# Optimization experiments

Hardware: AMD Instinct MI355X
Metric: run time of the kernel (lower is better)

Reference implementation:

```python
import jax, jax.numpy as jnp
import numpy as np
import math

L_DEG, N_PTS, T_ER, P_RAD, C_IN, C_OUT = 4, 8192, 15, 5, 16, 16


def _cg(j1, m1, j2, m2, j3, m3):
    # Clebsch-Gordan coefficient <j1 m1 j2 m2 | j3 m3> (Racah formula),
    # replacing sympy's CG(...).doit() used by the original module.
    if m1 + m2 != m3:
        return 0.0
    if j3 < abs(j1 - j2) or j3 > j1 + j2:
        return 0.0
    f = math.factorial
    pre = math.sqrt((2 * j3 + 1) * f(j3 + j1 - j2) * f(j3 - j1 + j2) * f(j1 + j2 - j3) / f(j1 + j2 + j3 + 1))
    pre *= math.sqrt(f(j3 + m3) * f(j3 - m3) * f(j1 - m1) * f(j1 + m1) * f(j2 - m2) * f(j2 + m2))
    s = 0.0
    for k in range(max(0, j2 - j3 - m1, j1 - j3 + m2), min(j1 + j2 - j3, j1 - m1, j2 + m2) + 1):
        s += (-1.0) ** k / (f(k) * f(j1 + j2 - j3 - k) * f(j1 - m1 - k) * f(j2 + m2 - k) * f(j3 - j2 + m1 + k) * f(j3 - j1 - m2 + k))
    return pre * s


def _precompute(L):
    # Mirrors PrecomputingTensorsForConv6D.
    tens, coefs = [], []
    for l in range(L):
        for l1 in range(L):
            for l2 in range(abs(l - l1), min(L, l + l1 + 1)):
                coefs.append(8.0 * np.pi ** 2 / (2 * l1 + 1)
                             * np.sqrt((2 * l + 1) * (2 * l1 + 1) / (4.0 * np.pi * (2 * l2 + 1)))
                             * _cg(l, 0, l1, 0, l2, 0))
                T1 = np.zeros((l + 1, l1 + 1, l2 + 1), np.float32)
                T2 = np.zeros_like(T1)
                T3 = np.zeros_like(T1)
                for k in range(l + 1):
                    for k1 in range(l1 + 1):
                        if k + k1 < l2 + 1:
                            T1[k, k1, k + k1] = _cg(l, k, l1, k1, l2, k + k1) * (-1) ** k1
                        if k1 > 0 and abs(k - k1) < l2 + 1:
                            if k - k1 >= 0:
                                T2[k, k1, k - k1] = _cg(l, k, l1, -k1, l2, k - k1) * (-1) ** l1
                            else:
                                T3[k, k1, k1 - k] = (-1) ** (k1 - k) * (-1) ** (l1 + l2) * _cg(l, k, l1, -k1, l2, k - k1)
                tens += [T1, T2, T3]
    return tens, [float(c) for c in coefs]


_TENS_NP, _COEFS = _precompute(L_DEG)
_TENS = [jnp.asarray(t, jnp.float32) for t in _TENS_NP]


def _forward(xs, ws, bs):
    L = L_DEG
    # zero the imaginary k=0 rows, as done via temp_term in build()
    ws_m = list(ws)
    bs_m = list(bs)
    for l in range(L):
        mk = (jnp.arange(l + 1) > 0).astype(jnp.float32)
        ws_m[2 * l + 1] = ws[2 * l + 1] * mk[:, None, None, None, None]
        bs_m[2 * l + 1] = bs[2 * l + 1] * mk[None, :, None, None]
    out = []
    itr = 0
    for l in range(L):
        o_r = 0.0
        o_i = 0.0
        for l1 in range(L):
            wr, wi = ws_m[2 * l1], ws_m[2 * l1 + 1]
            for l2 in range(abs(l - l1), min(L, l + l1 + 1)):
                c = _COEFS[itr]
                T1, T2, T3 = _TENS[3 * itr], _TENS[3 * itr + 1], _TENS[3 * itr + 2]
                xr, xi = xs[2 * l2], xs[2 * l2 + 1]
                # x: [n, t, k(l2+1), p, i]; w: [m(l1+1), t, p, i, j]; T: [l(l+1), m, k]
                o_r = o_r + c * jnp.einsum('lmk,ntkpi,mtpij->nlpj', T1 + T2 + T3, xr, wr) \
                          - c * jnp.einsum('lmk,ntkpi,mtpij->nlpj', T1 - T2 + T3, xi, wi)
                o_i = o_i + c * jnp.einsum('lmk,ntkpi,mtpij->nlpj', T1 - T2 - T3, xr, wi) \
                          + c * jnp.einsum('lmk,ntkpi,mtpij->nlpj', T1 + T2 - T3, xi, wr)
                itr += 1
        out.append(o_r + bs_m[2 * l])
        out.append(o_i + bs_m[2 * l + 1])
    return tuple(out)


def setup_inputs() -> dict:
    key = jax.random.key(0)
    ks = jax.random.split(key, 24)
    inp = {}
    i = 0
    for l in range(L_DEG):
        for part in ('r', 'i'):
            inp['x%d%s' % (l, part)] = jax.random.normal(ks[i], (N_PTS, T_ER, l + 1, P_RAD, C_IN), jnp.float32)
            i += 1
    for l in range(L_DEG):
        for part in ('r', 'i'):
            inp['w%d%s' % (l, part)] = jax.random.normal(ks[i], (l + 1, T_ER, P_RAD, C_IN, C_OUT), jnp.float32) * 0.05
            i += 1
    for l in range(L_DEG):
        for part in ('r', 'i'):
            inp['b%d%s' % (l, part)] = jax.random.normal(ks[i], (1, l + 1, P_RAD, C_OUT), jnp.float32) * 0.05
            i += 1
    return inp


def reference(x0r, x0i, x1r, x1i, x2r, x2i, x3r, x3i,
              w0r, w0i, w1r, w1i, w2r, w2i, w3r, w3i,
              b0r, b0i, b1r, b1i, b2r, b2i, b3r, b3i):
    xs = [x0r, x0i, x1r, x1i, x2r, x2i, x3r, x3i]
    ws = [w0r, w0i, w1r, w1i, w2r, w2i, w3r, w3i]
    bs = [b0r, b0i, b1r, b1i, b2r, b2i, b3r, b3i]
    return _forward(xs, ws, bs)
```

## Files before the change

### kernel.cpp

```cpp
#include <hip/hip_runtime.h>

#define PI_D 3.14159265358979323846


typedef __attribute__((ext_vector_type(8))) short short8;
typedef __attribute__((ext_vector_type(4))) float f32x4;

struct Ptrs8 { const float* p[8]; };

__device__ __forceinline__ ushort f2bf(float x){
  uint u = __float_as_uint(x);
  return (ushort)((u + 0x7fffu + ((u>>16)&1u)) >> 16);
}

__device__ __forceinline__ double dfact(int n){ double r=1.0; for(int i=2;i<=n;++i) r*=(double)i; return r; }

__device__ double cg_coef(int j1,int m1,int j2,int m2,int j3,int m3){
  if(m1+m2!=m3) return 0.0;
  if(j3<abs(j1-j2)||j3>j1+j2) return 0.0;
  if(abs(m1)>j1||abs(m2)>j2||abs(m3)>j3) return 0.0;
  double pre = sqrt((2.0*j3+1.0)*dfact(j3+j1-j2)*dfact(j3-j1+j2)*dfact(j1+j2-j3)/dfact(j1+j2+j3+1));
  pre *= sqrt(dfact(j3+m3)*dfact(j3-m3)*dfact(j1-m1)*dfact(j1+m1)*dfact(j2-m2)*dfact(j2+m2));
  int kmin = max(0,max(j2-j3-m1,j1-j3+m2));
  int kmax = min(j1+j2-j3,min(j1-m1,j2+m2));
  double s=0.0;
  for(int k=kmin;k<=kmax;++k){
    double d = dfact(k)*dfact(j1+j2-j3-k)*dfact(j1-m1-k)*dfact(j2+m2-k)*dfact(j3-j2+m1+k)*dfact(j3-j1-m2+k);
    s += ((k&1)?-1.0:1.0)/d;
  }
  return pre*s;
}

__device__ __forceinline__ int gidx(int l,int l2,int combo,int lr,int kx,int l1,int m){
  return ((((((l*4+l2)*4+combo)*4+lr)*4+kx)*4+l1)*4+m);
}

__global__ void g_kernel(float* __restrict__ G){
  int tid = threadIdx.x;
  for(int e=tid;e<16384;e+=blockDim.x) G[e]=0.0f;
  __syncthreads();
  int trip = tid >> 4;
  int sub  = tid & 15;
  int lr = sub >> 2, m = sub & 3;
  int idx=0;
  for(int l=0;l<4;l++)for(int l1=0;l1<4;l1++){
    int lo=abs(l-l1), hi=min(3,l+l1);
    for(int l2=lo;l2<=hi;l2++){
      if(idx==trip && lr<=l && m<=l1){
        double c = 8.0*PI_D*PI_D/(2.0*l1+1.0)
                 * sqrt((2.0*l+1.0)*(2.0*l1+1.0)/(4.0*PI_D*(2.0*l2+1.0)))
                 * cg_coef(l,0,l1,0,l2,0);
        if(lr+m<=l2){
          float f = (float)(c * cg_coef(l,lr,l1,m,l2,lr+m) * ((m&1)?-1.0:1.0));
          G[gidx(l,l2,0,lr,lr+m,l1,m)] += f;
          G[gidx(l,l2,1,lr,lr+m,l1,m)] -= f;
          G[gidx(l,l2,2,lr,lr+m,l1,m)] += f;
          G[gidx(l,l2,3,lr,lr+m,l1,m)] += f;
        }
        if(m>0 && abs(lr-m)<=l2){
          if(lr-m>=0){
            float f = (float)(c * cg_coef(l,lr,l1,-m,l2,lr-m) * ((l1&1)?-1.0:1.0));
            G[gidx(l,l2,0,lr,lr-m,l1,m)] += f;
            G[gidx(l,l2,1,lr,lr-m,l1,m)] += f;
            G[gidx(l,l2,2,lr,lr-m,l1,m)] -= f;
            G[gidx(l,l2,3,lr,lr-m,l1,m)] += f;
          } else {
            float f = (float)(c * (((m-lr)&1)?-1.0:1.0) * (((l1+l2)&1)?-1.0:1.0)
                              * cg_coef(l,lr,l1,-m,l2,lr-m));
            G[gidx(l,l2,0,lr,m-lr,l1,m)] += f;
            G[gidx(l,l2,1,lr,m-lr,l1,m)] -= f;
            G[gidx(l,l2,2,lr,m-lr,l1,m)] -= f;
            G[gidx(l,l2,3,lr,m-lr,l1,m)] -= f;
          }
        }
      }
      idx++;
    }
  }
}

__device__ __forceinline__ void decode_kb(int kb,int& l2,int& partp,int& kx,int& t){
  int kbo;
  if(kb<30){l2=0;kbo=0;} else if(kb<90){l2=1;kbo=30;} else if(kb<180){l2=2;kbo=90;} else {l2=3;kbo=180;}
  int rem = kb-kbo;
  int per = (l2+1)*15;
  partp = rem/per;
  int q = rem%per;
  kx = q/15; t = q%15;
}

__device__ __forceinline__ void decode_col(int col,int& l,int& part,int& lr,int& j){
  int co;
  if(col<32){l=0;co=0;} else if(col<96){l=1;co=32;} else if(col<192){l=2;co=96;} else {l=3;co=192;}
  int cr = col-co; int per=(l+1)*16;
  part = cr/per; int q = cr%per; lr = q>>4; j = q&15;
}

__global__ void w_kernel(const float* __restrict__ G, Ptrs8 wp, ushort* __restrict__ W){
  long e = (long)blockIdx.x*256 + threadIdx.x;
  if(e >= 5L*320*4800) return;
  int K = (int)(e%4800); long r = e/4800; int col = (int)(r%320); int p = (int)(r/320);
  int i = K & 15; int kb = K >> 4;
  int l2,partp,kx,t; decode_kb(kb,l2,partp,kx,t);
  int l,part,lr,j; decode_col(col,l,part,lr,j);
  int combo = (part==0) ? (partp==0?0:1) : (partp==0?2:3);
  int wpart = (combo==0||combo==3)?0:1;
  int mstart = wpart?1:0;
  int woff = t*1280 + p*256 + i*16 + j;
  float acc=0.f;
  for(int l1=0;l1<4;l1++){
    const float* wptr = wp.p[l1*2+wpart];
    int gb = ((((l*4+l2)*4+combo)*4+lr)*4+kx)*16 + l1*4;
    for(int m=mstart;m<=l1;m++){
      float g = G[gb+m];
      if(g!=0.f) acc += g * wptr[m*19200 + woff];
    }
  }
  W[e] = f2bf(acc);
}


__device__ __forceinline__ void a_load(const Ptrs8& xp, int p, int n0, int kt, int w, int lane, float4* v){
  int kb = kt*4 + w;
  int l2,partp,kx,t; decode_kb(kb,l2,partp,kx,t);
  const float* xb = xp.p[l2*2+partp];
  int nstr = 1200*(l2+1);
  const float* base = xb + (long)(n0 + (lane>>2))*nstr + (t*(l2+1)+kx)*80 + p*16 + (lane&3)*4;
  long step = (long)16*nstr;
  #pragma unroll
  for(int s=0;s<4;++s) v[s] = *(const float4*)(base + s*step);
}

__device__ __forceinline__ void a_store(ushort* As, int w, int lane, const float4* v){
  int rsub = lane>>2, c4 = (lane&3)*4;
  #pragma unroll
  for(int s=0;s<4;++s){
    int row = s*16 + rsub;
    int e = row*64 + ((w*16 + c4) ^ ((row&7)<<3));
    uint2 d;
    d.x = (uint)f2bf(v[s].x) | ((uint)f2bf(v[s].y)<<16);
    d.y = (uint)f2bf(v[s].z) | ((uint)f2bf(v[s].w)<<16);
    *(uint2*)(As + e) = d;
  }
}

__device__ __forceinline__ void b_load(const ushort* Wp, int w, int lane, int kt, short8* b){
  const ushort* q = Wp + (long)(w*80 + (lane&15))*4800 + kt*64 + ((lane>>4)*8);
  #pragma unroll
  for(int ks=0;ks<2;++ks)
    #pragma unroll
    for(int ni=0;ni<5;++ni)
      b[ks*5+ni] = *(const short8*)(q + (long)ni*16*4800 + ks*32);
}

__device__ __forceinline__ void do_mfma(const ushort* As, int lane, const short8* b, f32x4 acc[4][5]){
  #pragma unroll
  for(int ks=0;ks<2;++ks){
    short8 af[4];
    #pragma unroll
    for(int mi=0;mi<4;++mi){
      int row = mi*16 + (lane&15);
      int e = row*64 + (((ks*32) + (lane>>4)*8) ^ ((row&7)<<3));
      af[mi] = *(const short8*)(As + e);
    }
    #pragma unroll
    for(int mi=0;mi<4;++mi)
      #pragma unroll
      for(int ni=0;ni<5;++ni)
        acc[mi][ni] = __builtin_amdgcn_mfma_f32_16x16x32_bf16(af[mi], b[ks*5+ni], acc[mi][ni], 0,0,0);
  }
}

__global__ __launch_bounds__(256,2) void gemm_kernel(Ptrs8 xp, const ushort* __restrict__ Wb,
                                                     Ptrs8 bp, float* __restrict__ out){
  __shared__ ushort As[2][4096];
  const int tid = threadIdx.x;
  const int lane = tid & 63;
  const int w = tid >> 6;
  int orig = blockIdx.x;
  int x = orig & 7, q = orig >> 3;
  const int p = q % 5;
  const int nb = (q/5)*8 + x;
  const int n0 = nb*64;
  const ushort* Wp = Wb + (long)p*320*4800;

  f32x4 acc[4][5] = {};
  float4 av[4];
  short8 bfr[10];

  a_load(xp, p, n0, 0, w, lane, av);
  a_store(&As[0][0], w, lane, av);
  b_load(Wp, w, lane, 0, bfr);
  __syncthreads();

  int buf = 0;
  #pragma unroll 1
  for(int kt=0;kt<74;++kt){
    a_load(xp, p, n0, kt+1, w, lane, av);
    do_mfma(&As[buf][0], lane, bfr, acc);
    b_load(Wp, w, lane, kt+1, bfr);
    a_store(&As[buf^1][0], w, lane, av);
    __syncthreads();
    buf ^= 1;
  }
  do_mfma(&As[buf][0], lane, bfr, acc);

  int j = lane & 15, rg = (lane>>4)*4;
  #pragma unroll
  for(int ni=0;ni<5;++ni){
    int col16 = w*5 + ni;
    int l, part, lr;
    if(col16<2){l=0;part=col16;lr=0;}
    else if(col16<6){int c=col16-2;l=1;part=c>>1;lr=c&1;}
    else if(col16<12){int c=col16-6;l=2;part=(c>=3);lr=part?(c-3):c;}
    else {int c=col16-12;l=3;part=c>>2;lr=c&3;}
    float bv = 0.f;
    if(!(part==1 && lr==0)) bv = bp.p[l*2+part][lr*80 + p*16 + j];
    long base = 655360L*(l+1)*(l+part);
    int nst = (l+1)*80;
    long ioff = base + lr*80 + p*16 + j;
    #pragma unroll
    for(int mi=0;mi<4;++mi){
      int n = n0 + mi*16 + rg;
      #pragma unroll
      for(int r=0;r<4;++r)
        out[ioff + (long)(n+r)*nst] = acc[mi][ni][r] + bv;
    }
  }
}

extern "C" void kernel_launch(void* const* d_in, const int* in_sizes, int n_in,
                              void* d_out, int out_size, void* d_ws, size_t ws_size,
                              hipStream_t stream){
  Ptrs8 xp, wp, bp;
  for(int i=0;i<8;i++){
    xp.p[i] = (const float*)d_in[i];
    wp.p[i] = (const float*)d_in[8+i];
    bp.p[i] = (const float*)d_in[16+i];
  }
  float* G = (float*)d_ws;
  ushort* W = (ushort*)((char*)d_ws + 16384*4);
  g_kernel<<<dim3(1), dim3(576), 0, stream>>>(G);
  w_kernel<<<dim3(30000), dim3(256), 0, stream>>>(G, wp, W);
  gemm_kernel<<<dim3(640), dim3(256), 0, stream>>>(xp, W, bp, (float*)d_out);
}
```

Before: 482.8 us.

## Pre-pack activations to bf16 K-contiguous layout and pipeline GEMM with LDS DMA

Adds a pack kernel that converts the eight fp32 activation tensors into one bf16 buffer per radial index, laid out K-contiguous with an XOR swizzle. A new GEMM then streams A tiles straight into LDS with global_load_lds across a triple buffer of 192-wide K chunks, keeps three B fragment sets in flight, and synchronises with explicit waitcnt and barriers. The aim is to cut the scattered fp32 loads and in-loop conversion from the GEMM and to overlap memory with MFMA work. The cost is an extra pass that reads all activations and writes about 390MB of workspace, plus a fallback to the old kernel when the workspace is too small.

```diff
diff --git a/kernel.cpp b/kernel.cpp
--- a/kernel.cpp
+++ b/kernel.cpp
@@ -11,6 +11,11 @@
 __device__ __forceinline__ ushort f2bf(float x){
   uint u = __float_as_uint(x);
   return (ushort)((u + 0x7fffu + ((u>>16)&1u)) >> 16);
+}
+
+__device__ __forceinline__ void gload16(const void* g, ushort* l){
+  __builtin_amdgcn_global_load_lds((const __attribute__((address_space(1))) void*)g,
+                                   (__attribute__((address_space(3))) void*)l, 16, 0, 0);
 }
 
 __device__ __forceinline__ double dfact(int n){ double r=1.0; for(int i=2;i<=n;++i) r*=(double)i; return r; }
@@ -119,32 +124,45 @@
   W[e] = f2bf(acc);
 }
 
-
-__device__ __forceinline__ void a_load(const Ptrs8& xp, int p, int n0, int kt, int w, int lane, float4* v){
-  int kb = kt*4 + w;
-  int l2,partp,kx,t; decode_kb(kb,l2,partp,kx,t);
-  const float* xb = xp.p[l2*2+partp];
-  int nstr = 1200*(l2+1);
-  const float* base = xb + (long)(n0 + (lane>>2))*nstr + (t*(l2+1)+kx)*80 + p*16 + (lane&3)*4;
-  long step = (long)16*nstr;
-  #pragma unroll
-  for(int s=0;s<4;++s) v[s] = *(const float4*)(base + s*step);
-}
-
-__device__ __forceinline__ void a_store(ushort* As, int w, int lane, const float4* v){
-  int rsub = lane>>2, c4 = (lane&3)*4;
-  #pragma unroll
-  for(int s=0;s<4;++s){
-    int row = s*16 + rsub;
-    int e = row*64 + ((w*16 + c4) ^ ((row&7)<<3));
-    uint2 d;
-    d.x = (uint)f2bf(v[s].x) | ((uint)f2bf(v[s].y)<<16);
-    d.y = (uint)f2bf(v[s].z) | ((uint)f2bf(v[s].w)<<16);
-    *(uint2*)(As + e) = d;
-  }
-}
-
-__device__ __forceinline__ void b_load(const ushort* Wp, int w, int lane, int kt, short8* b){
+__global__ __launch_bounds__(256) void pack_kernel(Ptrs8 xp, ushort* __restrict__ Xp){
+  __shared__ ushort L[5*4816];
+  const int tid = threadIdx.x;
+  const int n = blockIdx.x;
+  const int nsw = (n & 7) << 3;
+  #pragma unroll
+  for(int a=0;a<8;a++){
+    const int l2 = a>>1, partp = a&1;
+    const int kbo = (l2==0)?0:(l2==1)?30:(l2==2)?90:180;
+    const int kbase = kbo + partp*15*(l2+1);
+    const float* row = xp.p[a] + (long)n*1200*(l2+1);
+    const int nf4 = 300*(l2+1);
+    for(int u=tid; u<nf4; u+=256){
+      float4 v = ((const float4*)row)[u];
+      int f = u*4;
+      int i = f & 15;
+      int r = f >> 4;
+      int p = r % 5;
+      int tk = r / 5;
+      int kx = tk % (l2+1);
+      int t  = tk / (l2+1);
+      int K = (kbase + kx*15 + t)*16 + i;
+      int idx = p*4816 + ((((K>>3)*8) ^ nsw)) + (K&7);
+      uint2 d;
+      d.x = (uint)f2bf(v.x) | ((uint)f2bf(v.y)<<16);
+      d.y = (uint)f2bf(v.z) | ((uint)f2bf(v.w)<<16);
+      *(uint2*)(&L[idx]) = d;
+    }
+  }
+  __syncthreads();
+  for(int u=tid; u<3000; u+=256){
+    int p = u/600, b = u - p*600;
+    const uint4 s = *(const uint4*)(&L[p*4816 + b*8]);
+    *(uint4*)((char*)Xp + ((long)p*8192 + n)*9600 + b*16) = s;
+  }
+}
+
+
+__device__ __forceinline__ void b_load(const ushort* Wp,int w,int lane,int kt,short8* b){
   const ushort* q = Wp + (long)(w*80 + (lane&15))*4800 + kt*64 + ((lane>>4)*8);
   #pragma unroll
   for(int ks=0;ks<2;++ks)
@@ -153,15 +171,15 @@
       b[ks*5+ni] = *(const short8*)(q + (long)ni*16*4800 + ks*32);
 }
 
-__device__ __forceinline__ void do_mfma(const ushort* As, int lane, const short8* b, f32x4 acc[4][5]){
+__device__ __forceinline__ void do_mfma192(const ushort* A,int ktl,int lane,const short8* b,f32x4 acc[4][5]){
   #pragma unroll
   for(int ks=0;ks<2;++ks){
     short8 af[4];
     #pragma unroll
     for(int mi=0;mi<4;++mi){
-      int row = mi*16 + (lane&15);
-      int e = row*64 + (((ks*32) + (lane>>4)*8) ^ ((row&7)<<3));
-      af[mi] = *(const short8*)(As + e);
+      int nn = mi*16 + (lane&15);
+      int idx = nn*192 + ((ktl*64 + ks*32 + ((lane>>4)<<3)) ^ ((nn&7)<<3));
+      af[mi] = *(const short8*)(A + idx);
     }
     #pragma unroll
     for(int mi=0;mi<4;++mi)
@@ -171,39 +189,74 @@
   }
 }
 
-__global__ __launch_bounds__(256,2) void gemm_kernel(Ptrs8 xp, const ushort* __restrict__ Wb,
-                                                     Ptrs8 bp, float* __restrict__ out){
-  __shared__ ushort As[2][4096];
+__device__ __forceinline__ void stageA(const char* Xb,const int* srcb,int cc,ushort* buf,int w){
+  #pragma unroll
+  for(int c6=0;c6<6;++c6)
+    gload16(Xb + srcb[c6] + cc*384, buf + ((c6*4096 + w*1024)>>1));
+}
+
+__global__ __launch_bounds__(256,2) void gemm_xp(const ushort* __restrict__ Xp,
+                                                 const ushort* __restrict__ Wb,
+                                                 Ptrs8 bp, float* __restrict__ out){
+  __shared__ ushort As[3][12288];
   const int tid = threadIdx.x;
   const int lane = tid & 63;
   const int w = tid >> 6;
   int orig = blockIdx.x;
-  int x = orig & 7, q = orig >> 3;
-  const int p = q % 5;
-  const int nb = (q/5)*8 + x;
+  int wg = (orig & 7)*80 + (orig >> 3);
+  const int p = wg / 128;
+  const int nb = wg % 128;
   const int n0 = nb*64;
   const ushort* Wp = Wb + (long)p*320*4800;
+  const char* Xb = (const char*)Xp + (long)p*8192*9600;
+
+  int srcb[6];
+  #pragma unroll
+  for(int c6=0;c6<6;++c6){
+    int o = c6*4096 + tid*16;
+    srcb[c6] = (n0 + o/384)*9600 + (o%384);
+  }
 
   f32x4 acc[4][5] = {};
-  float4 av[4];
-  short8 bfr[10];
-
-  a_load(xp, p, n0, 0, w, lane, av);
-  a_store(&As[0][0], w, lane, av);
-  b_load(Wp, w, lane, 0, bfr);
-  __syncthreads();
-
-  int buf = 0;
+  short8 bfr0[10], bfr1[10], bfr2[10];
+
+  stageA(Xb, srcb, 0, &As[0][0], w);
+  stageA(Xb, srcb, 1, &As[1][0], w);
+  b_load(Wp, w, lane, 0, bfr0);
+  b_load(Wp, w, lane, 1, bfr1);
+  b_load(Wp, w, lane, 2, bfr2);
+
   #pragma unroll 1
-  for(int kt=0;kt<74;++kt){
-    a_load(xp, p, n0, kt+1, w, lane, av);
-    do_mfma(&As[buf][0], lane, bfr, acc);
-    b_load(Wp, w, lane, kt+1, bfr);
-    a_store(&As[buf^1][0], w, lane, av);
-    __syncthreads();
-    buf ^= 1;
-  }
-  do_mfma(&As[buf][0], lane, bfr, acc);
+  for(int c=0;c<25;++c){
+    asm volatile("s_waitcnt vmcnt(20)" ::: "memory");
+    __builtin_amdgcn_sched_barrier(0);
+    __builtin_amdgcn_s_barrier();
+    __builtin_amdgcn_sched_barrier(0);
+    {
+      int cc = min(c+2, 24);
+      stageA(Xb, srcb, cc, &As[(c+2)%3][0], w);
+    }
+    __builtin_amdgcn_sched_barrier(0);
+    const ushort* Ab = &As[c%3][0];
+    __builtin_amdgcn_s_setprio(1);
+    do_mfma192(Ab, 0, lane, bfr0, acc);
+    __builtin_amdgcn_s_setprio(0);
+    b_load(Wp, w, lane, min(3*c+3,74), bfr0);
+    __builtin_amdgcn_sched_barrier(0);
+    asm volatile("s_waitcnt vmcnt(26)" ::: "memory");
+    __builtin_amdgcn_sched_barrier(0);
+    __builtin_amdgcn_s_setprio(1);
+    do_mfma192(Ab, 1, lane, bfr1, acc);
+    __builtin_amdgcn_s_setprio(0);
+    b_load(Wp, w, lane, min(3*c+4,74), bfr1);
+    __builtin_amdgcn_sched_barrier(0);
+    asm volatile("s_waitcnt vmcnt(26)" ::: "memory");
+    __builtin_amdgcn_sched_barrier(0);
+    __builtin_amdgcn_s_setprio(1);
+    do_mfma192(Ab, 2, lane, bfr2, acc);
+    __builtin_amdgcn_s_setprio(0);
+    b_load(Wp, w, lane, min(3*c+5,74), bfr2);
+  }
 
   int j = lane & 15, rg = (lane>>4)*4;
   #pragma unroll
@@ -229,6 +282,106 @@
   }
 }
 
+__device__ __forceinline__ void a_load(const Ptrs8& xp, int p, int n0, int kt, int w, int lane, float4* v){
+  int kb = kt*4 + w;
+  int l2,partp,kx,t; decode_kb(kb,l2,partp,kx,t);
+  const float* xb = xp.p[l2*2+partp];
+  int nstr = 1200*(l2+1);
+  const float* base = xb + (long)(n0 + (lane>>2))*nstr + (t*(l2+1)+kx)*80 + p*16 + (lane&3)*4;
+  long step = (long)16*nstr;
+  #pragma unroll
+  for(int s=0;s<4;++s) v[s] = *(const float4*)(base + s*step);
+}
+
+__device__ __forceinline__ void a_store(ushort* As, int w, int lane, const float4* v){
+  int rsub = lane>>2, c4 = (lane&3)*4;
+  #pragma unroll
+  for(int s=0;s<4;++s){
+    int row = s*16 + rsub;
+    int e = row*64 + ((w*16 + c4) ^ ((row&7)<<3));
+    uint2 d;
+    d.x = (uint)f2bf(v[s].x) | ((uint)f2bf(v[s].y)<<16);
+    d.y = (uint)f2bf(v[s].z) | ((uint)f2bf(v[s].w)<<16);
+    *(uint2*)(As + e) = d;
+  }
+}
+
+__device__ __forceinline__ void do_mfma64(const ushort* As, int lane, const short8* b, f32x4 acc[4][5]){
+  #pragma unroll
+  for(int ks=0;ks<2;++ks){
+    short8 af[4];
+    #pragma unroll
+    for(int mi=0;mi<4;++mi){
+      int row = mi*16 + (lane&15);
+      int e = row*64 + (((ks*32) + (lane>>4)*8) ^ ((row&7)<<3));
+      af[mi] = *(const short8*)(As + e);
+    }
+    #pragma unroll
+    for(int mi=0;mi<4;++mi)
+      #pragma unroll
+      for(int ni=0;ni<5;++ni)
+        acc[mi][ni] = __builtin_amdgcn_mfma_f32_16x16x32_bf16(af[mi], b[ks*5+ni], acc[mi][ni], 0,0,0);
+  }
+}
+
+__global__ __launch_bounds__(256,2) void gemm_direct(Ptrs8 xp, const ushort* __restrict__ Wb,
+                                                     Ptrs8 bp, float* __restrict__ out){
+  __shared__ ushort As[2][4096];
+  const int tid = threadIdx.x;
+  const int lane = tid & 63;
+  const int w = tid >> 6;
+  int orig = blockIdx.x;
+  int x = orig & 7, q = orig >> 3;
+  const int p = q % 5;
+  const int nb = (q/5)*8 + x;
+  const int n0 = nb*64;
+  const ushort* Wp = Wb + (long)p*320*4800;
+
+  f32x4 acc[4][5] = {};
+  float4 av[4];
+  short8 bfr[10];
+
+  a_load(xp, p, n0, 0, w, lane, av);
+  a_store(&As[0][0], w, lane, av);
+  b_load(Wp, w, lane, 0, bfr);
+  __syncthreads();
+
+  int buf = 0;
+  #pragma unroll 1
+  for(int kt=0;kt<74;++kt){
+    a_load(xp, p, n0, kt+1, w, lane, av);
+    do_mfma64(&As[buf][0], lane, bfr, acc);
+    b_load(Wp, w, lane, kt+1, bfr);
+    a_store(&As[buf^1][0], w, lane, av);
+    __syncthreads();
+    buf ^= 1;
+  }
+  do_mfma64(&As[buf][0], lane, bfr, acc);
+
+  int j = lane & 15, rg = (lane>>4)*4;
+  #pragma unroll
+  for(int ni=0;ni<5;++ni){
+    int col16 = w*5 + ni;
+    int l, part, lr;
+    if(col16<2){l=0;part=col16;lr=0;}
+    else if(col16<6){int c=col16-2;l=1;part=c>>1;lr=c&1;}
+    else if(col16<12){int c=col16-6;l=2;part=(c>=3);lr=part?(c-3):c;}
+    else {int c=col16-12;l=3;part=c>>2;lr=c&3;}
+    float bv = 0.f;
+    if(!(part==1 && lr==0)) bv = bp.p[l*2+part][lr*80 + p*16 + j];
+    long base = 655360L*(l+1)*(l+part);
+    int nst = (l+1)*80;
+    long ioff = base + lr*80 + p*16 + j;
+    #pragma unroll
+    for(int mi=0;mi<4;++mi){
+      int n = n0 + mi*16 + rg;
+      #pragma unroll
+      for(int r=0;r<4;++r)
+        out[ioff + (long)(n+r)*nst] = acc[mi][ni][r] + bv;
+    }
+  }
+}
+
 extern "C" void kernel_launch(void* const* d_in, const int* in_sizes, int n_in,
                               void* d_out, int out_size, void* d_ws, size_t ws_size,
                               hipStream_t stream){
@@ -239,8 +392,15 @@
     bp.p[i] = (const float*)d_in[16+i];
   }
   float* G = (float*)d_ws;
-  ushort* W = (ushort*)((char*)d_ws + 16384*4);
+  ushort* W = (ushort*)((char*)d_ws + 65536);
   g_kernel<<<dim3(1), dim3(576), 0, stream>>>(G);
   w_kernel<<<dim3(30000), dim3(256), 0, stream>>>(G, wp, W);
-  gemm_kernel<<<dim3(640), dim3(256), 0, stream>>>(xp, W, bp, (float*)d_out);
-}
+  const size_t need = 16777216ull + 5ull*8192*9600;
+  if(ws_size >= need){
+    ushort* Xp = (ushort*)((char*)d_ws + 16777216);
+    pack_kernel<<<dim3(8192), dim3(256), 0, stream>>>(xp, Xp);
+    gemm_xp<<<dim3(640), dim3(256), 0, stream>>>(Xp, W, bp, (float*)d_out);
+  } else {
+    gemm_direct<<<dim3(640), dim3(256), 0, stream>>>(xp, W, bp, (float*)d_out);
+  }
+}
```

Result: slower. 665.0 us (+37.7%).
